# Kernel optimization log

Measured on AMD Instinct MI355X. Metric: run time of the kernel, lower is better.

## Reference

```python
import jax, jax.numpy as jnp
import numpy as np
from jax import lax

VDECAY, VTH, GRAD_WIN, GRAD_AMP = 0.5, 0.5, 0.5, 1.0

@jax.custom_vjp
def spike(v):
    return (v > VTH).astype(v.dtype)

def _spike_fwd(v):
    return spike(v), v

def _spike_bwd(v, g):
    # rectangular surrogate gradient
    win = (jnp.abs(v - VTH) <= GRAD_WIN).astype(g.dtype)
    return (GRAD_AMP * g * win,)

spike.defvjp(_spike_fwd, _spike_bwd)

def setup_inputs() -> dict:
    key = jax.random.key(0)
    ks = jax.random.split(key, 3)
    B, D_IN, T, H, D_OUT = 256, 700, 250, 1024, 20
    spike_data = (jax.random.uniform(ks[0], (B, D_IN, T)) < 0.1).astype(jnp.float32)
    W_hid = jax.random.normal(ks[1], (H, D_IN), dtype=jnp.float32) * (1.0 / np.sqrt(D_IN))
    W_out = jax.random.normal(ks[2], (D_OUT, H), dtype=jnp.float32) * (1.0 / np.sqrt(H))
    return {
        "spike_data": spike_data,
        "W_hid": W_hid,
        "W_out": W_out,
        "hid_spike0": jnp.zeros((B, H), jnp.float32),
        "hid_volt0": jnp.zeros((B, H), jnp.float32),
        "out_spike0": jnp.zeros((B, D_OUT), jnp.float32),
        "out_volt0": jnp.zeros((B, D_OUT), jnp.float32),
        "batch_size": 256,
        "spike_ts": 250,
    }

def reference(spike_data, W_hid, W_out, hid_spike0, hid_volt0, out_spike0, out_volt0, batch_size, spike_ts):
    # [B, D_in, T] -> [T, B, D_in] for scan over time
    xs = jnp.moveaxis(spike_data.reshape(batch_size, -1, spike_ts), -1, 0)

    def step(carry, s_in):
        hs, hv, os_, ov = carry
        hv = hv * VDECAY * (1.0 - hs) + s_in @ W_hid.T      # leaky integrate, reset on spike
        hs = spike(hv)                                       # hidden spikes
        ov = ov * VDECAY * (1.0 - os_) + hs @ W_out.T
        os_ = spike(ov)
        return (hs, hv, os_, ov), os_

    _, out_spikes = lax.scan(step, (hid_spike0, hid_volt0, out_spike0, out_volt0), xs)
    return jnp.sum(out_spikes, axis=0)  # [B, D_out] spike counts
```

## Files before the change

kernel.cpp:

```cpp
#include <hip/hip_runtime.h>
#include <stdint.h>

#define B      256
#define DIN    700
#define T      250
#define H      1024
#define DOUT   20
#define NW_IN  11
#define NW_INP 12
#define NW_H   16
#define LMAX   160
#define JSENT2 22512

typedef unsigned long long u64;

__global__ void prep_weights(const float* __restrict__ W_hid,
                             const float* __restrict__ W_out,
                             float* __restrict__ Wt,
                             float* __restrict__ WoT) {
    int idx = blockIdx.x * 256 + threadIdx.x;
    if (blockIdx.x < 2800) {
        int d = idx / H;
        int h = idx - d * H;
        Wt[idx] = W_hid[h * DIN + d];
    } else {
        int i = idx - 2800 * 256;
        int h = i / DOUT;
        int o = i - h * DOUT;
        WoT[i] = W_out[o * H + h];
    }
}

__global__ void prep_bits(const float* __restrict__ spk,
                          u64* __restrict__ bits) {
    int b  = blockIdx.x >> 2;
    int wc = blockIdx.x & 3;
    int t  = threadIdx.x;
    if (t >= T) return;
    int w0 = wc * 3;
    int w1 = (wc == 3) ? NW_IN : w0 + 3;
    const float* base = spk + (size_t)b * DIN * T + t;
    for (int w = w0; w < w1; ++w) {
        u64 m = 0;
#pragma unroll
        for (int j = 0; j < 64; ++j) {
            int d = (w << 6) + j;
            if (d < DIN) {
                float x = base[(size_t)d * T];
                m |= (u64)(x > 0.5f) << j;
            }
        }
        bits[((size_t)b * T + t) * NW_INP + w] = m;
    }
}

__global__ void __launch_bounds__(256)
prep_lists2(const u64* __restrict__ bits,
            unsigned short* __restrict__ lists,
            unsigned* __restrict__ nrow) {
    __shared__ unsigned short scr[4][LMAX];

    int wv   = threadIdx.x >> 6;
    int lane = threadIdx.x & 63;
    int row  = blockIdx.x * 4 + wv;

    const u64* wp = bits + (size_t)row * NW_INP;
    u64 mw = (lane < NW_IN) ? wp[lane] : 0ull;

    for (int i = lane; i < LMAX; i += 64) scr[wv][i] = (unsigned short)JSENT2;

    u64 lowmask = (1ull << lane) - 1ull;
    int pos = 0;
    unsigned counts = 0;

#pragma unroll
    for (int p = 0; p < 4; ++p) {
        int jlo = 175 * p, jhi = jlo + 175;
        int n = 0;
        for (int k = jlo >> 6; k <= (jhi - 1) >> 6; ++k) {
            u64 m = __shfl(mw, k);
            int lo = jlo - (k << 6);
            int hi = jhi - (k << 6);
            if (lo > 0)  m &= ~((1ull << lo) - 1ull);
            if (hi < 64) m &= (1ull << hi) - 1ull;
            if ((m >> lane) & 1ull) {
                int q = pos + n + __popcll(m & lowmask);
                int jl = (k << 6) + lane - jlo;
                if (q < LMAX)
                    scr[wv][q] = (unsigned short)(jl * 128 + ((jl & 7) << 4));
            }
            n += __popcll(m);
        }
        int c = (n + 3) >> 2;
        counts |= (unsigned)c << (8 * p);
        pos += c * 4;
    }

    if (lane == 0) nrow[row] = counts;
    __syncthreads();

    const unsigned* s32 = (const unsigned*)scr[wv];
    unsigned* g32 = (unsigned*)(lists + (size_t)row * LMAX);
    g32[lane] = s32[lane];
    if (lane < 16) g32[64 + lane] = s32[64 + lane];
}

__global__ void __launch_bounds__(256)
sort_rows(const unsigned* __restrict__ nrow,
          unsigned char* __restrict__ perm) {
    __shared__ int cnt[8][32];
    __shared__ int off[8][32];
    int b = blockIdx.x, tid = threadIdx.x;
    cnt[tid >> 5][tid & 31] = 0;
    __syncthreads();
    unsigned cc = 0; int half = 0, lt = 0;
    if (tid < T) {
        cc = nrow[b * T + tid];
        half = tid >= 125;
        lt = tid - half * 125;
#pragma unroll
        for (int p = 0; p < 4; ++p) {
            int c = (cc >> (8 * p)) & 0xff; if (c > 31) c = 31;
            atomicAdd(&cnt[p * 2 + half][c], 1);
        }
    }
    __syncthreads();
    if (tid < 8) {
        int s = 0;
        for (int i = 0; i < 32; ++i) { off[tid][i] = s; s += cnt[tid][i]; cnt[tid][i] = 0; }
    }
    __syncthreads();
    if (tid < T) {
#pragma unroll
        for (int p = 0; p < 4; ++p) {
            int c = (cc >> (8 * p)) & 0xff; if (c > 31) c = 31;
            int sidx = p * 2 + half;
            int rank = off[sidx][c] + atomicAdd(&cnt[sidx][c], 1);
            perm[((size_t)b * 8 + sidx) * 128 + rank] = (unsigned char)lt;
        }
    }
}

__global__ void __launch_bounds__(512, 8)
hidden_slice3(const unsigned short* __restrict__ lists,
              const unsigned* __restrict__ nrow,
              const unsigned char* __restrict__ perm,
              const float* __restrict__ Wt,
              const float* __restrict__ hs0,
              const float* __restrict__ hv0,
              u64* __restrict__ hsbits) {
    __shared__ float wlds[176 * 32];
    __shared__ float cur[125 * 32];

    int s    = blockIdx.x;
    int b    = blockIdx.y;
    int tid  = threadIdx.x;
    int wv   = tid >> 6;
    int lane = tid & 63;
    int g    = lane >> 3;
    int li   = lane & 7;
    int lxor = li << 4;
    int l    = lane & 31;

    float keep = 0.0f;
    if (wv == 0) {
        int h = s * 32 + l;
        keep = hv0[b * H + h] * 0.5f * (1.0f - hs0[b * H + h]);
    }
    unsigned* hp = (unsigned*)hsbits;

    for (int th = 0; th < 2; ++th) {
        for (int p = 0; p < 4; ++p) {
            {
                int jr  = tid >> 3;
                int lis = tid & 7;
#pragma unroll
                for (int bj = 0; bj < 192; bj += 64) {
                    int jl = bj + jr;
                    if (jl < 176) {
                        float4 v = make_float4(0.0f, 0.0f, 0.0f, 0.0f);
                        if (jl < 175)
                            v = *(const float4*)(Wt + (size_t)(p * 175 + jl) * H + s * 32 + lis * 4);
                        *(float4*)((char*)wlds + jl * 128 + ((lis ^ (jl & 7)) << 4)) = v;
                    }
                }
            }
            __syncthreads();

            const unsigned char* pm = perm + ((size_t)b * 8 + p * 2 + th) * 128;

#pragma unroll
            for (int sweep = 0; sweep < 2; ++sweep) {
                int rr = sweep * 64 + wv * 8 + g;
                if (rr < 125) {
                    int lr  = pm[rr];
                    int r   = th * 125 + lr;
                    int row = b * T + r;
                    unsigned cc = nrow[row];
                    int c = (cc >> (8 * p)) & 0xff;
                    int offc = 0;
                    if (p > 0) offc += (cc & 0xff);
                    if (p > 1) offc += ((cc >> 8) & 0xff);
                    if (p > 2) offc += ((cc >> 16) & 0xff);
                    const uint2* qp = (const uint2*)(lists + (size_t)row * LMAX + offc * 4);
                    char* cp = (char*)cur + lr * 128 + ((li ^ (lr & 7)) << 4);

                    float a0, a1, a2, a3;
                    if (p == 0) {
                        a0 = a1 = a2 = a3 = 0.0f;
                    } else {
                        float4 cv = *(const float4*)cp;
                        a0 = cv.x; a1 = cv.y; a2 = cv.z; a3 = cv.w;
                    }

                    if (c > 0) {
                        uint2 w2 = qp[0];
                        int ch = 0;
                        for (;;) {
                            uint2 nw = (ch + 1 < c) ? qp[ch + 1] : w2;
                            int e0 = w2.x & 0xffff, e1 = w2.x >> 16;
                            int e2 = w2.y & 0xffff, e3 = w2.y >> 16;
                            float4 v0 = *(const float4*)((char*)wlds + (e0 ^ lxor));
                            float4 v1 = *(const float4*)((char*)wlds + (e1 ^ lxor));
                            float4 v2 = *(const float4*)((char*)wlds + (e2 ^ lxor));
                            float4 v3 = *(const float4*)((char*)wlds + (e3 ^ lxor));
                            a0 += v0.x; a1 += v0.y; a2 += v0.z; a3 += v0.w;
                            a0 += v1.x; a1 += v1.y; a2 += v1.z; a3 += v1.w;
                            a0 += v2.x; a1 += v2.y; a2 += v2.z; a3 += v2.w;
                            a0 += v3.x; a1 += v3.y; a2 += v3.z; a3 += v3.w;
                            ++ch;
                            if (ch >= c) break;
                            w2 = nw;
                        }
                    }
                    float4 o; o.x = a0; o.y = a1; o.z = a2; o.w = a3;
                    *(float4*)cp = o;
                }
            }
            __syncthreads();
        }

        if (wv == 0) {
            for (int lt = 0; lt < 125; ++lt) {
                float cv = *(const float*)((char*)cur + lt * 128 +
                                           (((l >> 2) ^ (lt & 7)) << 4) + (l & 3) * 4);
                float hv = keep + cv;
                bool sp = hv > 0.5f;
                keep = sp ? 0.0f : hv * 0.5f;
                u64 ball = __ballot(sp);
                int t = th * 125 + lt;
                if (lane == 0)
                    hp[(size_t)(b * T + t) * 32 + s] = (unsigned)ball;
            }
        }
        __syncthreads();
    }
}

__global__ void __launch_bounds__(1024)
hidden_fused(const u64* __restrict__ bits,
             const float* __restrict__ Wt,
             const float* __restrict__ hs0,
             const float* __restrict__ hv0,
             u64* __restrict__ hsbits) {
    __shared__ int idx_l[2][256];

    int b = blockIdx.x;
    int h = threadIdx.x;
    int wv   = h >> 6;
    int lane = h & 63;

    float keep = hv0[b * H + h] * 0.5f * (1.0f - hs0[b * H + h]);

    const u64* bb = bits + (size_t)b * T * NW_INP;

    for (int t = 0; t < T; ++t) {
        const u64* wp = bb + (size_t)t * NW_INP;
        u64 w[NW_IN];
#pragma unroll
        for (int k = 0; k < NW_IN; ++k) w[k] = wp[k];

        int base[NW_IN + 1];
        base[0] = 0;
#pragma unroll
        for (int k = 0; k < NW_IN; ++k) base[k + 1] = base[k] + __popcll(w[k]);
        int n = base[NW_IN];

        int buf = t & 1;
        if (wv < NW_IN) {
            u64 m = w[wv];
            if ((m >> lane) & 1ull) {
                int pos = base[wv] + __popcll(m & ((1ull << lane) - 1ull));
                idx_l[buf][pos] = (wv << 6) + lane;
            }
        }
        __syncthreads();

        const int* il = idx_l[buf];
        float cur2 = 0.0f;
        int i = 0;
        for (; i + 8 <= n; i += 8) {
            int j0 = il[i + 0], j1 = il[i + 1], j2 = il[i + 2], j3 = il[i + 3];
            int j4 = il[i + 4], j5 = il[i + 5], j6 = il[i + 6], j7 = il[i + 7];
            float v0 = Wt[(size_t)j0 * H + h];
            float v1 = Wt[(size_t)j1 * H + h];
            float v2 = Wt[(size_t)j2 * H + h];
            float v3 = Wt[(size_t)j3 * H + h];
            float v4 = Wt[(size_t)j4 * H + h];
            float v5 = Wt[(size_t)j5 * H + h];
            float v6 = Wt[(size_t)j6 * H + h];
            float v7 = Wt[(size_t)j7 * H + h];
            cur2 += v0; cur2 += v1; cur2 += v2; cur2 += v3;
            cur2 += v4; cur2 += v5; cur2 += v6; cur2 += v7;
        }
        for (; i < n; ++i) cur2 += Wt[(size_t)il[i] * H + h];

        float hv = keep + cur2;
        bool sp = hv > 0.5f;
        keep = sp ? 0.0f : hv * 0.5f;
        u64 ball = __ballot(sp);
        if (lane == 0)
            hsbits[((size_t)b * T + t) * NW_H + wv] = ball;
    }
}

__global__ void __launch_bounds__(512)
out_currents2(const u64* __restrict__ hsbits,
              const float* __restrict__ WoT,
              float* __restrict__ Iout) {
    __shared__ float wot[H * DOUT];

    int tid = threadIdx.x;
    {
        const float4* src = (const float4*)WoT;
        float4* dst = (float4*)wot;
#pragma unroll
        for (int k = 0; k < 10; ++k)
            dst[k * 512 + tid] = src[k * 512 + tid];
    }
    __syncthreads();

    int wv   = tid >> 6;
    int lane = tid & 63;
    int sub  = lane / 20;
    int o    = lane - sub * 20;
    int row  = blockIdx.x * 24 + wv * 3 + sub;
    if (sub >= 3 || row >= B * T) return;

    const u64* wp = hsbits + (size_t)row * NW_H;
    u64 w[NW_H];
#pragma unroll
    for (int k = 0; k < NW_H; ++k) w[k] = wp[k];

    float acc = 0.0f;
#pragma unroll
    for (int k = 0; k < NW_H; ++k) {
        u64 m = w[k];
        const float* base = wot + k * 64 * DOUT + o;
        while (m) {
            int h0 = __builtin_ctzll(m);
            m &= m - 1;
            acc += base[h0 * DOUT];
        }
    }
    Iout[(size_t)row * DOUT + o] = acc;
}

__global__ void __launch_bounds__(256)
out_scan(const float* __restrict__ Iout,
         const float* __restrict__ os0,
         const float* __restrict__ ov0,
         float* __restrict__ outp) {
    __shared__ float pan[T * DOUT];

    int b   = blockIdx.x;
    int tid = threadIdx.x;

    const float* src = Iout + (size_t)b * T * DOUT;
#pragma unroll
    for (int k = 0; k < 20; ++k) {
        int i = k * 256 + tid;
        if (i < T * DOUT) pan[i] = src[i];
    }
    __syncthreads();

    if (tid < DOUT) {
        int o = tid;
        int idx = b * DOUT + o;
        float ov = ov0[idx];
        float os = os0[idx];
        float keep = ov * 0.5f * (1.0f - os);
        float cnt = 0.0f;
#pragma unroll 5
        for (int t = 0; t < T; ++t) {
            float v = keep + pan[t * DOUT + o];
            float sp = (v > 0.5f) ? 1.0f : 0.0f;
            cnt += sp;
            keep = v * 0.5f * (1.0f - sp);
        }
        outp[idx] = cnt;
    }
}

extern "C" void kernel_launch(void* const* d_in, const int* in_sizes, int n_in,
                              void* d_out, int out_size, void* d_ws, size_t ws_size,
                              hipStream_t stream) {
    const float* spike = (const float*)d_in[0];
    const float* W_hid = (const float*)d_in[1];
    const float* W_out = (const float*)d_in[2];
    const float* hs0   = (const float*)d_in[3];
    const float* hv0   = (const float*)d_in[4];
    const float* os0   = (const float*)d_in[5];
    const float* ov0   = (const float*)d_in[6];
    float* outp = (float*)d_out;

    char* ws = (char*)d_ws;
    float*          Wt     = (float*)(ws);
    float*          WoT    = (float*)(ws + 2867200);
    u64*            bits   = (u64*)  (ws + 2949120);
    u64*            hsbits = (u64*)  (ws + 9093120);
    float*          Iout   = (float*)(ws + 17285120);
    unsigned short* lists  = (unsigned short*)(ws + 22405120);
    unsigned*       nrow   = (unsigned*)(ws + 42885120);
    unsigned char*  perm   = (unsigned char*)(ws + 43141120);
    const size_t need = 43403264;

    prep_weights<<<2880, 256, 0, stream>>>(W_hid, W_out, Wt, WoT);
    prep_bits<<<1024, 256, 0, stream>>>(spike, bits);

    if (ws_size >= need) {
        prep_lists2<<<16000, 256, 0, stream>>>(bits, lists, nrow);
        sort_rows<<<B, 256, 0, stream>>>(nrow, perm);
        hidden_slice3<<<dim3(32, 256), 512, 0, stream>>>(lists, nrow, perm, Wt, hs0, hv0, hsbits);
    } else {
        hidden_fused<<<B, 1024, 0, stream>>>(bits, Wt, hs0, hv0, hsbits);
    }

    out_currents2<<<2667, 512, 0, stream>>>(hsbits, WoT, Iout);
    out_scan<<<B, 256, 0, stream>>>(Iout, os0, ov0, outp);
}
```

Measured before the change: 965.4 us.

## Read second half of hidden weights from global memory instead of LDS staging

For input chunks p=2,3 the hidden kernel stops staging weight tiles into shared memory and gathers float4 weight rows straight from global (L2-cached) memory, using raw input indices stored in the spike lists. A zero padding row at index 700 is added to Wt so that padding entries in the lists are harmless, and the workspace offsets are shifted to make room for it. This removes two of the four LDS tile loads and their barriers per time half, in exchange for higher-latency global gathers in the inner loop.

```diff
diff --git a/kernel.cpp b/kernel.cpp
--- a/kernel.cpp
+++ b/kernel.cpp
@@ -23,11 +23,14 @@
         int d = idx / H;
         int h = idx - d * H;
         Wt[idx] = W_hid[h * DIN + d];
-    } else {
+    } else if (blockIdx.x < 2880) {
         int i = idx - 2800 * 256;
         int h = i / DOUT;
         int o = i - h * DOUT;
         WoT[i] = W_out[o * H + h];
+    } else {
+        int i2 = idx - 2880 * 256;
+        if (i2 < H) Wt[700 * H + i2] = 0.0f;
     }
 }
 
@@ -85,13 +88,21 @@
             if (hi < 64) m &= (1ull << hi) - 1ull;
             if ((m >> lane) & 1ull) {
                 int q = pos + n + __popcll(m & lowmask);
-                int jl = (k << 6) + lane - jlo;
-                if (q < LMAX)
-                    scr[wv][q] = (unsigned short)(jl * 128 + ((jl & 7) << 4));
+                if (q < LMAX) {
+                    int j  = (k << 6) + lane;
+                    int jl = j - jlo;
+                    scr[wv][q] = (p < 2)
+                        ? (unsigned short)(jl * 128 + ((jl & 7) << 4))
+                        : (unsigned short)j;
+                }
             }
             n += __popcll(m);
         }
         int c = (n + 3) >> 2;
+        if (p >= 2 && lane < 3) {
+            int q = pos + n + lane;
+            if (q < pos + c * 4 && q < LMAX) scr[wv][q] = 700;
+        }
         counts |= (unsigned)c << (8 * p);
         pos += c * 4;
     }
@@ -162,6 +173,8 @@
     int lxor = li << 4;
     int l    = lane & 31;
 
+    const char* wtb = (const char*)Wt + s * 128 + li * 16;
+
     float keep = 0.0f;
     if (wv == 0) {
         int h = s * 32 + l;
@@ -170,8 +183,9 @@
     unsigned* hp = (unsigned*)hsbits;
 
     for (int th = 0; th < 2; ++th) {
+#pragma unroll
         for (int p = 0; p < 4; ++p) {
-            {
+            if (p < 2) {
                 int jr  = tid >> 3;
                 int lis = tid & 7;
 #pragma unroll
@@ -184,8 +198,8 @@
                         *(float4*)((char*)wlds + jl * 128 + ((lis ^ (jl & 7)) << 4)) = v;
                     }
                 }
-            }
-            __syncthreads();
+                __syncthreads();
+            }
 
             const unsigned char* pm = perm + ((size_t)b * 8 + p * 2 + th) * 128;
 
@@ -220,10 +234,18 @@
                             uint2 nw = (ch + 1 < c) ? qp[ch + 1] : w2;
                             int e0 = w2.x & 0xffff, e1 = w2.x >> 16;
                             int e2 = w2.y & 0xffff, e3 = w2.y >> 16;
-                            float4 v0 = *(const float4*)((char*)wlds + (e0 ^ lxor));
-                            float4 v1 = *(const float4*)((char*)wlds + (e1 ^ lxor));
-                            float4 v2 = *(const float4*)((char*)wlds + (e2 ^ lxor));
-                            float4 v3 = *(const float4*)((char*)wlds + (e3 ^ lxor));
+                            float4 v0, v1, v2, v3;
+                            if (p < 2) {
+                                v0 = *(const float4*)((char*)wlds + (e0 ^ lxor));
+                                v1 = *(const float4*)((char*)wlds + (e1 ^ lxor));
+                                v2 = *(const float4*)((char*)wlds + (e2 ^ lxor));
+                                v3 = *(const float4*)((char*)wlds + (e3 ^ lxor));
+                            } else {
+                                v0 = *(const float4*)(wtb + ((size_t)e0 << 12));
+                                v1 = *(const float4*)(wtb + ((size_t)e1 << 12));
+                                v2 = *(const float4*)(wtb + ((size_t)e2 << 12));
+                                v3 = *(const float4*)(wtb + ((size_t)e3 << 12));
+                            }
                             a0 += v0.x; a1 += v0.y; a2 += v0.z; a3 += v0.w;
                             a0 += v1.x; a1 += v1.y; a2 += v1.z; a3 += v1.w;
                             a0 += v2.x; a1 += v2.y; a2 += v2.z; a3 += v2.w;
@@ -416,16 +438,16 @@
 
     char* ws = (char*)d_ws;
     float*          Wt     = (float*)(ws);
-    float*          WoT    = (float*)(ws + 2867200);
-    u64*            bits   = (u64*)  (ws + 2949120);
-    u64*            hsbits = (u64*)  (ws + 9093120);
-    float*          Iout   = (float*)(ws + 17285120);
-    unsigned short* lists  = (unsigned short*)(ws + 22405120);
-    unsigned*       nrow   = (unsigned*)(ws + 42885120);
-    unsigned char*  perm   = (unsigned char*)(ws + 43141120);
-    const size_t need = 43403264;
-
-    prep_weights<<<2880, 256, 0, stream>>>(W_hid, W_out, Wt, WoT);
+    float*          WoT    = (float*)(ws + 2871296);
+    u64*            bits   = (u64*)  (ws + 2953216);
+    u64*            hsbits = (u64*)  (ws + 9097216);
+    float*          Iout   = (float*)(ws + 17289216);
+    unsigned short* lists  = (unsigned short*)(ws + 22409216);
+    unsigned*       nrow   = (unsigned*)(ws + 42889216);
+    unsigned char*  perm   = (unsigned char*)(ws + 43145216);
+    const size_t need = 43407360;
+
+    prep_weights<<<2896, 256, 0, stream>>>(W_hid, W_out, Wt, WoT);
     prep_bits<<<1024, 256, 0, stream>>>(spike, bits);
 
     if (ws_size >= need) {
```

After: 1.353 ms. 1.4x slower.

## Split input dimension into two halves and process all timesteps per block

Applied to the files above, without the earlier changes.

The hidden-current kernel now stages 352-row halves of the weight slice in LDS instead of 175-row quarters, and handles all 250 timesteps in one pass. This halves the number of weight reloads and barriers, and runs the voltage scan once at the end. The per-row metadata, sorting and list layout are reworked to match: two chunk counts packed in a ushort, and perm holds 256 entries per half. In exchange LDS use per block roughly doubles (about 77KB), so occupancy drops and the launch bound changes from 8 to 4 waves.

```diff
diff --git a/kernel.cpp b/kernel.cpp
--- a/kernel.cpp
+++ b/kernel.cpp
@@ -10,7 +10,7 @@
 #define NW_INP 12
 #define NW_H   16
 #define LMAX   160
-#define JSENT2 22512
+#define JSENT  45056
 
 typedef unsigned long long u64;
 
@@ -57,7 +57,7 @@
 __global__ void __launch_bounds__(256)
 prep_lists2(const u64* __restrict__ bits,
             unsigned short* __restrict__ lists,
-            unsigned* __restrict__ nrow) {
+            unsigned short* __restrict__ nrow) {
     __shared__ unsigned short scr[4][LMAX];
 
     int wv   = threadIdx.x >> 6;
@@ -67,36 +67,42 @@
     const u64* wp = bits + (size_t)row * NW_INP;
     u64 mw = (lane < NW_IN) ? wp[lane] : 0ull;
 
-    for (int i = lane; i < LMAX; i += 64) scr[wv][i] = (unsigned short)JSENT2;
+    for (int i = lane; i < LMAX; i += 64) scr[wv][i] = (unsigned short)JSENT;
 
     u64 lowmask = (1ull << lane) - 1ull;
-    int pos = 0;
-    unsigned counts = 0;
-
-#pragma unroll
-    for (int p = 0; p < 4; ++p) {
-        int jlo = 175 * p, jhi = jlo + 175;
-        int n = 0;
-        for (int k = jlo >> 6; k <= (jhi - 1) >> 6; ++k) {
-            u64 m = __shfl(mw, k);
-            int lo = jlo - (k << 6);
-            int hi = jhi - (k << 6);
-            if (lo > 0)  m &= ~((1ull << lo) - 1ull);
-            if (hi < 64) m &= (1ull << hi) - 1ull;
-            if ((m >> lane) & 1ull) {
-                int q = pos + n + __popcll(m & lowmask);
-                int jl = (k << 6) + lane - jlo;
-                if (q < LMAX)
-                    scr[wv][q] = (unsigned short)(jl * 128 + ((jl & 7) << 4));
-            }
-            n += __popcll(m);
-        }
-        int c = (n + 3) >> 2;
-        counts |= (unsigned)c << (8 * p);
-        pos += c * 4;
-    }
-
-    if (lane == 0) nrow[row] = counts;
+
+    int nA = 0;
+#pragma unroll
+    for (int k = 0; k < 6; ++k) {
+        u64 m = __shfl(mw, k);
+        if (k == 5) m &= 0xffffffffull;
+        if ((m >> lane) & 1ull) {
+            int pos = nA + __popcll(m & lowmask);
+            int j = (k << 6) + lane;
+            if (pos < LMAX)
+                scr[wv][pos] = (unsigned short)(j * 128 + ((j & 7) << 4));
+        }
+        nA += __popcll(m);
+    }
+    int cA = (nA + 3) >> 2;
+    int bs = cA * 4;
+
+    int nB = 0;
+#pragma unroll
+    for (int k = 5; k < NW_IN; ++k) {
+        u64 m = __shfl(mw, k);
+        if (k == 5) m &= ~0xffffffffull;
+        if ((m >> lane) & 1ull) {
+            int pos = bs + nB + __popcll(m & lowmask);
+            int jl = (k << 6) + lane - 352;
+            if (pos < LMAX)
+                scr[wv][pos] = (unsigned short)(jl * 128 + ((jl & 7) << 4));
+        }
+        nB += __popcll(m);
+    }
+    int cB = (nB + 3) >> 2;
+
+    if (lane == 0) nrow[row] = (unsigned short)(cA | (cB << 8));
     __syncthreads();
 
     const unsigned* s32 = (const unsigned*)scr[wv];
@@ -106,51 +112,44 @@
 }
 
 __global__ void __launch_bounds__(256)
-sort_rows(const unsigned* __restrict__ nrow,
+sort_rows(const unsigned short* __restrict__ nrow,
           unsigned char* __restrict__ perm) {
-    __shared__ int cnt[8][32];
-    __shared__ int off[8][32];
+    __shared__ int cnt[2][32], off[2][32];
     int b = blockIdx.x, tid = threadIdx.x;
-    cnt[tid >> 5][tid & 31] = 0;
-    __syncthreads();
-    unsigned cc = 0; int half = 0, lt = 0;
+    if (tid < 64) cnt[tid >> 5][tid & 31] = 0;
+    __syncthreads();
+    int cA = 0, cB = 0;
     if (tid < T) {
-        cc = nrow[b * T + tid];
-        half = tid >= 125;
-        lt = tid - half * 125;
-#pragma unroll
-        for (int p = 0; p < 4; ++p) {
-            int c = (cc >> (8 * p)) & 0xff; if (c > 31) c = 31;
-            atomicAdd(&cnt[p * 2 + half][c], 1);
-        }
-    }
-    __syncthreads();
-    if (tid < 8) {
+        unsigned cc = nrow[b * T + tid];
+        cA = cc & 0xff;          if (cA > 31) cA = 31;
+        cB = (cc >> 8) & 0xff;   if (cB > 31) cB = 31;
+        atomicAdd(&cnt[0][cA], 1);
+        atomicAdd(&cnt[1][cB], 1);
+    }
+    __syncthreads();
+    if (tid < 2) {
         int s = 0;
         for (int i = 0; i < 32; ++i) { off[tid][i] = s; s += cnt[tid][i]; cnt[tid][i] = 0; }
     }
     __syncthreads();
     if (tid < T) {
-#pragma unroll
-        for (int p = 0; p < 4; ++p) {
-            int c = (cc >> (8 * p)) & 0xff; if (c > 31) c = 31;
-            int sidx = p * 2 + half;
-            int rank = off[sidx][c] + atomicAdd(&cnt[sidx][c], 1);
-            perm[((size_t)b * 8 + sidx) * 128 + rank] = (unsigned char)lt;
-        }
-    }
-}
-
-__global__ void __launch_bounds__(512, 8)
-hidden_slice3(const unsigned short* __restrict__ lists,
-              const unsigned* __restrict__ nrow,
+        int rA = off[0][cA] + atomicAdd(&cnt[0][cA], 1);
+        int rB = off[1][cB] + atomicAdd(&cnt[1][cB], 1);
+        perm[((size_t)b * 2 + 0) * 256 + rA] = (unsigned char)tid;
+        perm[((size_t)b * 2 + 1) * 256 + rB] = (unsigned char)tid;
+    }
+}
+
+__global__ void __launch_bounds__(512, 4)
+hidden_slice4(const unsigned short* __restrict__ lists,
+              const unsigned short* __restrict__ nrow,
               const unsigned char* __restrict__ perm,
               const float* __restrict__ Wt,
               const float* __restrict__ hs0,
               const float* __restrict__ hv0,
               u64* __restrict__ hsbits) {
-    __shared__ float wlds[176 * 32];
-    __shared__ float cur[125 * 32];
+    __shared__ float wlds[353 * 32];
+    __shared__ float cur[250 * 32];
 
     int s    = blockIdx.x;
     int b    = blockIdx.y;
@@ -169,91 +168,84 @@
     }
     unsigned* hp = (unsigned*)hsbits;
 
-    for (int th = 0; th < 2; ++th) {
-        for (int p = 0; p < 4; ++p) {
-            {
-                int jr  = tid >> 3;
-                int lis = tid & 7;
-#pragma unroll
-                for (int bj = 0; bj < 192; bj += 64) {
-                    int jl = bj + jr;
-                    if (jl < 176) {
-                        float4 v = make_float4(0.0f, 0.0f, 0.0f, 0.0f);
-                        if (jl < 175)
-                            v = *(const float4*)(Wt + (size_t)(p * 175 + jl) * H + s * 32 + lis * 4);
-                        *(float4*)((char*)wlds + jl * 128 + ((lis ^ (jl & 7)) << 4)) = v;
+    for (int p = 0; p < 2; ++p) {
+        {
+            int jr  = tid >> 3;
+            int lis = tid & 7;
+            int lim = p ? 348 : 352;
+#pragma unroll
+            for (int bj = 0; bj < 384; bj += 64) {
+                int jl = bj + jr;
+                if (jl < 353) {
+                    float4 v = make_float4(0.0f, 0.0f, 0.0f, 0.0f);
+                    if (jl < lim)
+                        v = *(const float4*)(Wt + (size_t)(p * 352 + jl) * H + s * 32 + lis * 4);
+                    *(float4*)((char*)wlds + jl * 128 + ((lis ^ (jl & 7)) << 4)) = v;
+                }
+            }
+        }
+        __syncthreads();
+
+        const unsigned char* pm = perm + ((size_t)b * 2 + p) * 256;
+
+#pragma unroll
+        for (int sweep = 0; sweep < 4; ++sweep) {
+            int rr = sweep * 64 + wv * 8 + g;
+            if (rr < 250) {
+                int t   = pm[rr];
+                int row = b * T + t;
+                unsigned cc = nrow[row];
+                int cA = cc & 0xff;
+                int c  = p ? ((cc >> 8) & 0xff) : cA;
+                const uint2* qp = (const uint2*)(lists + (size_t)row * LMAX + (p ? cA * 4 : 0));
+                char* cp = (char*)cur + t * 128 + ((li ^ (t & 7)) << 4);
+
+                float a0, a1, a2, a3;
+                if (p == 0) {
+                    a0 = a1 = a2 = a3 = 0.0f;
+                } else {
+                    float4 cv = *(const float4*)cp;
+                    a0 = cv.x; a1 = cv.y; a2 = cv.z; a3 = cv.w;
+                }
+
+                if (c > 0) {
+                    uint2 w2 = qp[0];
+                    int ch = 0;
+                    for (;;) {
+                        uint2 nw = (ch + 1 < c) ? qp[ch + 1] : w2;
+                        int e0 = w2.x & 0xffff, e1 = w2.x >> 16;
+                        int e2 = w2.y & 0xffff, e3 = w2.y >> 16;
+                        float4 v0 = *(const float4*)((char*)wlds + (e0 ^ lxor));
+                        float4 v1 = *(const float4*)((char*)wlds + (e1 ^ lxor));
+                        float4 v2 = *(const float4*)((char*)wlds + (e2 ^ lxor));
+                        float4 v3 = *(const float4*)((char*)wlds + (e3 ^ lxor));
+                        a0 += v0.x; a1 += v0.y; a2 += v0.z; a3 += v0.w;
+                        a0 += v1.x; a1 += v1.y; a2 += v1.z; a3 += v1.w;
+                        a0 += v2.x; a1 += v2.y; a2 += v2.z; a3 += v2.w;
+                        a0 += v3.x; a1 += v3.y; a2 += v3.z; a3 += v3.w;
+                        ++ch;
+                        if (ch >= c) break;
+                        w2 = nw;
                     }
                 }
+                float4 o; o.x = a0; o.y = a1; o.z = a2; o.w = a3;
+                *(float4*)cp = o;
             }
-            __syncthreads();
-
-            const unsigned char* pm = perm + ((size_t)b * 8 + p * 2 + th) * 128;
-
-#pragma unroll
-            for (int sweep = 0; sweep < 2; ++sweep) {
-                int rr = sweep * 64 + wv * 8 + g;
-                if (rr < 125) {
-                    int lr  = pm[rr];
-                    int r   = th * 125 + lr;
-                    int row = b * T + r;
-                    unsigned cc = nrow[row];
-                    int c = (cc >> (8 * p)) & 0xff;
-                    int offc = 0;
-                    if (p > 0) offc += (cc & 0xff);
-                    if (p > 1) offc += ((cc >> 8) & 0xff);
-                    if (p > 2) offc += ((cc >> 16) & 0xff);
-                    const uint2* qp = (const uint2*)(lists + (size_t)row * LMAX + offc * 4);
-                    char* cp = (char*)cur + lr * 128 + ((li ^ (lr & 7)) << 4);
-
-                    float a0, a1, a2, a3;
-                    if (p == 0) {
-                        a0 = a1 = a2 = a3 = 0.0f;
-                    } else {
-                        float4 cv = *(const float4*)cp;
-                        a0 = cv.x; a1 = cv.y; a2 = cv.z; a3 = cv.w;
-                    }
-
-                    if (c > 0) {
-                        uint2 w2 = qp[0];
-                        int ch = 0;
-                        for (;;) {
-                            uint2 nw = (ch + 1 < c) ? qp[ch + 1] : w2;
-                            int e0 = w2.x & 0xffff, e1 = w2.x >> 16;
-                            int e2 = w2.y & 0xffff, e3 = w2.y >> 16;
-                            float4 v0 = *(const float4*)((char*)wlds + (e0 ^ lxor));
-                            float4 v1 = *(const float4*)((char*)wlds + (e1 ^ lxor));
-                            float4 v2 = *(const float4*)((char*)wlds + (e2 ^ lxor));
-                            float4 v3 = *(const float4*)((char*)wlds + (e3 ^ lxor));
-                            a0 += v0.x; a1 += v0.y; a2 += v0.z; a3 += v0.w;
-                            a0 += v1.x; a1 += v1.y; a2 += v1.z; a3 += v1.w;
-                            a0 += v2.x; a1 += v2.y; a2 += v2.z; a3 += v2.w;
-                            a0 += v3.x; a1 += v3.y; a2 += v3.z; a3 += v3.w;
-                            ++ch;
-                            if (ch >= c) break;
-                            w2 = nw;
-                        }
-                    }
-                    float4 o; o.x = a0; o.y = a1; o.z = a2; o.w = a3;
-                    *(float4*)cp = o;
-                }
-            }
-            __syncthreads();
-        }
-
-        if (wv == 0) {
-            for (int lt = 0; lt < 125; ++lt) {
-                float cv = *(const float*)((char*)cur + lt * 128 +
-                                           (((l >> 2) ^ (lt & 7)) << 4) + (l & 3) * 4);
-                float hv = keep + cv;
-                bool sp = hv > 0.5f;
-                keep = sp ? 0.0f : hv * 0.5f;
-                u64 ball = __ballot(sp);
-                int t = th * 125 + lt;
-                if (lane == 0)
-                    hp[(size_t)(b * T + t) * 32 + s] = (unsigned)ball;
-            }
         }
         __syncthreads();
+    }
+
+    if (wv == 0) {
+        for (int t = 0; t < T; ++t) {
+            float cv = *(const float*)((char*)cur + t * 128 +
+                                       (((l >> 2) ^ (t & 7)) << 4) + (l & 3) * 4);
+            float hv = keep + cv;
+            bool sp = hv > 0.5f;
+            keep = sp ? 0.0f : hv * 0.5f;
+            u64 ball = __ballot(sp);
+            if (lane == 0)
+                hp[(size_t)(b * T + t) * 32 + s] = (unsigned)ball;
+        }
     }
 }
 
@@ -421,9 +413,9 @@
     u64*            hsbits = (u64*)  (ws + 9093120);
     float*          Iout   = (float*)(ws + 17285120);
     unsigned short* lists  = (unsigned short*)(ws + 22405120);
-    unsigned*       nrow   = (unsigned*)(ws + 42885120);
-    unsigned char*  perm   = (unsigned char*)(ws + 43141120);
-    const size_t need = 43403264;
+    unsigned short* nrow   = (unsigned short*)(ws + 42885120);
+    unsigned char*  perm   = (unsigned char*)(ws + 43013120);
+    const size_t need = 43144192;
 
     prep_weights<<<2880, 256, 0, stream>>>(W_hid, W_out, Wt, WoT);
     prep_bits<<<1024, 256, 0, stream>>>(spike, bits);
@@ -431,7 +423,7 @@
     if (ws_size >= need) {
         prep_lists2<<<16000, 256, 0, stream>>>(bits, lists, nrow);
         sort_rows<<<B, 256, 0, stream>>>(nrow, perm);
-        hidden_slice3<<<dim3(32, 256), 512, 0, stream>>>(lists, nrow, perm, Wt, hs0, hv0, hsbits);
+        hidden_slice4<<<dim3(32, 256), 512, 0, stream>>>(lists, nrow, perm, Wt, hs0, hv0, hsbits);
     } else {
         hidden_fused<<<B, 1024, 0, stream>>>(bits, Wt, hs0, hv0, hsbits);
     }
```

After: 1.159 ms. +20.1%, slower.
